# Performance work log

Hardware: AMD Instinct MI355X
Metric: run time of the kernel (lower is better)

## Reference

```python
import jax, jax.numpy as jnp
import numpy as np

B, L, C, D, M = 64, 256, 8, 512, 512


def setup_inputs() -> dict:
    key = jax.random.key(0)
    ks = jax.random.split(key, 12)
    sd = 1.0 / np.sqrt(D)
    sm = 1.0 / np.sqrt(M)
    return {
        "x": jax.random.normal(ks[0], (B, L, D), jnp.float32),
        "x_c": jax.random.randint(ks[1], (B, L, C), 0, L),
        "x_m": jax.random.uniform(ks[2], (B, L), jnp.float32),
        "x_m_c": jax.random.uniform(ks[3], (B, L, C), jnp.float32),
        "W_ioux": jax.random.uniform(ks[4], (3 * M, D), jnp.float32, -sd, sd),
        "b_ioux": jax.random.uniform(ks[5], (3 * M,), jnp.float32, -sd, sd),
        "W_iouh": jax.random.uniform(ks[6], (3 * M, M), jnp.float32, -sm, sm),
        "b_iouh": jax.random.uniform(ks[7], (3 * M,), jnp.float32, -sm, sm),
        "W_fx": jax.random.uniform(ks[8], (M, D), jnp.float32, -sd, sd),
        "b_fx": jax.random.uniform(ks[9], (M,), jnp.float32, -sd, sd),
        "W_fh": jax.random.uniform(ks[10], (M, M), jnp.float32, -sm, sm),
        "b_fh": jax.random.uniform(ks[11], (M,), jnp.float32, -sm, sm),
    }


def reference(x, x_c, x_m, x_m_c, W_ioux, b_ioux, W_iouh, b_iouh, W_fx, b_fx, W_fh, b_fh):
    bsz, len_seq, in_dim = x.shape
    mem = W_fx.shape[0]
    outputs0 = jnp.zeros((bsz, len_seq, 2 * mem), x.dtype)  # row 0 = init_state = zeros
    prev0 = jnp.zeros((bsz, 2 * mem), x.dtype)
    # time-major streams for steps 1..L-1
    xs = (
        jnp.arange(1, len_seq),
        jnp.swapaxes(x, 0, 1)[1:],
        jnp.swapaxes(x_c, 0, 1)[1:],
        jnp.swapaxes(x_m, 0, 1)[1:],
        jnp.swapaxes(x_m_c, 0, 1)[1:],
    )

    def step(carry, inputs):
        outputs, prev = carry
        t, x_t, xc_t, xm_t, xmc_t = inputs
        # gather child states [B, C, 2M] from outputs buffer
        idx = jnp.broadcast_to(xc_t[:, :, None], (bsz, xc_t.shape[1], 2 * mem))
        child = jnp.take_along_axis(outputs, idx, axis=1)
        c_s, c_h = child[..., :mem], child[..., mem:]
        mc = xmc_t[..., None]  # [B, C, 1]
        child_h_sum = jnp.sum(c_h * mc, axis=1)  # [B, M]
        iou = x_t @ W_ioux.T + b_ioux + child_h_sum @ W_iouh.T + b_iouh
        i, o, u = jnp.split(iou, 3, axis=-1)
        i, o, u = jax.nn.sigmoid(i), jax.nn.sigmoid(o), jnp.tanh(u)
        f = jax.nn.sigmoid(c_h @ W_fh.T + b_fh + (x_t @ W_fx.T + b_fx)[:, None, :])
        c = i * u + jnp.sum(f * c_s * mc, axis=1)
        h = o * jnp.tanh(c)
        s = jnp.concatenate([c, h], axis=-1)
        m = xm_t[:, None]
        s = m * s + (1.0 - m) * prev
        outputs = jax.lax.dynamic_update_slice(outputs, s[:, None, :], (0, t, 0))
        return (outputs, s), None

    (outputs, final_state), _ = jax.lax.scan(step, (outputs0, prev0), xs)
    return outputs, final_state
```

## Files before the change

### kernel.cpp

```cpp
#include <hip/hip_runtime.h>
#include <math.h>

namespace {

constexpr int Bn = 64, Ln = 256, Cn = 8, Dn = 512, Mn = 512;
constexpr int TWO_M = 2 * Mn;
constexpr int PCOLS = 2048;
constexpr size_t P_FLOATS = (size_t)Bn * Ln * PCOLS;
constexpr size_t P_BYTES  = P_FLOATS * 4;

__device__ __forceinline__ float sigmoidf_(float v) { return 1.0f / (1.0f + __expf(-v)); }
__device__ __forceinline__ float dot4_(float4 a, float4 b) {
    return a.x * b.x + a.y * b.y + a.z * b.z + a.w * b.w;
}

constexpr int PJLD = 36;

__global__ __launch_bounds__(256)
void proj2_kernel(const float* __restrict__ x,
                  const float* __restrict__ W_ioux, const float* __restrict__ b_ioux,
                  const float* __restrict__ b_iouh,
                  const float* __restrict__ W_fx, const float* __restrict__ b_fx,
                  float* __restrict__ P)
{
    __shared__ float sA[64 * PJLD];
    __shared__ float sB[64 * PJLD];
    const int tid = threadIdx.x;
    const int rb = blockIdx.x >> 5;
    const int cb = blockIdx.x & 31;
    const int r0 = rb * 64, c0 = cb * 64;
    const bool is_iou = (c0 < 3 * Mn);
    const int ri = tid & 15, ci = tid >> 4;

    float acc[4][4];
    #pragma unroll
    for (int r = 0; r < 4; ++r)
        #pragma unroll
        for (int c = 0; c < 4; ++c) acc[r][c] = 0.f;

    for (int k0 = 0; k0 < Dn; k0 += 32) {
        #pragma unroll
        for (int i = 0; i < 2; ++i) {
            const int flat = i * 256 + tid;
            const int row = flat >> 3, kq = flat & 7;
            *(float4*)&sA[row * PJLD + kq * 4] =
                *(const float4*)&x[(size_t)(r0 + row) * Dn + k0 + kq * 4];
            const float* wsrc = is_iou ? &W_ioux[(size_t)(c0 + row) * Dn]
                                       : &W_fx[(size_t)(c0 - 3 * Mn + row) * Dn];
            *(float4*)&sB[row * PJLD + kq * 4] = *(const float4*)&wsrc[k0 + kq * 4];
        }
        __syncthreads();
        #pragma unroll
        for (int k4 = 0; k4 < 8; ++k4) {
            float4 av[4], bv[4];
            #pragma unroll
            for (int r = 0; r < 4; ++r) av[r] = *(const float4*)&sA[(ri + r * 16) * PJLD + k4 * 4];
            #pragma unroll
            for (int c = 0; c < 4; ++c) bv[c] = *(const float4*)&sB[(ci + c * 16) * PJLD + k4 * 4];
            #pragma unroll
            for (int r = 0; r < 4; ++r)
                #pragma unroll
                for (int c = 0; c < 4; ++c) acc[r][c] += dot4_(av[r], bv[c]);
        }
        __syncthreads();
    }
    #pragma unroll
    for (int c = 0; c < 4; ++c) {
        const int col = c0 + ci + c * 16;
        const float bias = is_iou ? (b_ioux[col] + b_iouh[col]) : b_fx[col - 3 * Mn];
        #pragma unroll
        for (int r = 0; r < 4; ++r)
            P[(size_t)(r0 + ri + r * 16) * PCOLS + col] = acc[r][c] + bias;
    }
}

constexpr int R_W2  = 0;
constexpr int R_W1  = R_W2 + 8192;
constexpr int R_HS  = R_W1 + 24576;
constexpr int R_FD  = R_HS + 4096;
constexpr int R_IO  = R_FD + 1024;
constexpr int R_CS  = R_IO + 384;
constexpr int R_PV  = R_CS + 1024;
constexpr int R_XMC = R_PV + 256;
constexpr int R_XM  = R_XMC + 64;
constexpr int R_RB  = R_XM + 8;
constexpr int R_FLOATS = R_RB + 64;
constexpr size_t R_LDS_BYTES = (size_t)R_FLOATS * 4;
static_assert(R_LDS_BYTES <= 163840, "persist7 LDS over budget");

__global__ __launch_bounds__(512, 1)
void persist7_kernel(const int* __restrict__ x_c, const float* __restrict__ x_m,
                     const float* __restrict__ x_m_c,
                     const float* __restrict__ W_iouh, const float* __restrict__ W_fh,
                     const float* __restrict__ b_fh, const float* __restrict__ P,
                     float* __restrict__ out, unsigned* __restrict__ ctr)
{
    extern __shared__ float lds[];
    float* w2   = lds + R_W2;
    float* w1   = lds + R_W1;
    float* s_hs = lds + R_HS;
    float* s_fd = lds + R_FD;
    float* s_io = lds + R_IO;
    float* s_cs = lds + R_CS;
    float* s_pv = lds + R_PV;
    float* s_xmc = lds + R_XMC;
    float* s_xm  = lds + R_XM;
    int*   s_rb  = (int*)(lds + R_RB);

    const int tid = threadIdx.x;
    const int g  = blockIdx.x & 7;
    const int mt = blockIdx.x >> 3;
    const int m0 = mt * 16;
    const int b0 = g * 8;
    unsigned* myctr = ctr + g * 32;

    #pragma unroll
    for (int chk = 0; chk < 4; ++chk) {
        const int q = chk * 512 + tid;
        const int i = q >> 7, jj = (q >> 5) & 3, lane32 = q & 31;
        const int jh = lane32 >> 3, ks = lane32 & 7;
        *(float4*)&w2[q * 4] =
            *(const float4*)&W_fh[(size_t)(m0 + jh * 4 + jj) * Dn + ks * 4 + i * 32];
    }
    #pragma unroll
    for (int chk = 0; chk < 12; ++chk) {
        const int q = chk * 512 + tid;
        const int i = q / 384, r1 = q % 384;
        const int cc = r1 / 192, lane192 = r1 % 192;
        const int cq = lane192 >> 3, ks = lane192 & 7;
        const int col = cq * 2 + cc, s = col >> 4, j = col & 15;
        *(float4*)&w1[q * 4] =
            *(const float4*)&W_iouh[(size_t)(s * Mn + m0 + j) * Mn + ks * 4 + i * 32];
    }

    const int g2_ks = tid & 7, g2_jh = (tid >> 3) & 3, g2_rq = tid >> 5;
    const int g1_bq = tid / 192, g1_r = tid % 192;
    const int g1_cq = g1_r >> 3, g1_ks = g1_r & 7;
    const int p1_b = tid >> 6, p1_k = tid & 63;

    const float bfh_j = b_fh[m0 + (tid & 15)];
    if (tid < 256) s_pv[tid] = 0.f;

    int   sc_idx = 0;  float sc_xmc = 0.f, sc_xm = 0.f;
    float p0 = 0.f, p1 = 0.f, p2 = 0.f, p3 = 0.f;
    if (tid < 64) {
        const int b = tid >> 3, c = tid & 7;
        sc_idx = x_c[((size_t)(b0 + b) * Ln + 1) * Cn + c];
        sc_xmc = x_m_c[((size_t)(b0 + b) * Ln + 1) * Cn + c];
    } else if (tid < 72) {
        sc_xm = x_m[(size_t)(b0 + tid - 64) * Ln + 1];
    }
    if (tid < 128) {
        const size_t prow = ((size_t)(b0 + (tid >> 4)) * Ln + 1) * (size_t)PCOLS
                            + m0 + (tid & 15);
        p0 = P[prow];           p1 = P[prow + Mn];
        p2 = P[prow + 2 * Mn];  p3 = P[prow + 3 * Mn];
    }
    __syncthreads();

    for (int t = 1; t < Ln; ++t) {
        if (tid < 64) {
            const int ci = (sc_idx < t) ? sc_idx : 0;
            s_xmc[tid] = sc_xmc;
            s_rb[tid]  = ((b0 + (tid >> 3)) * Ln + ci) * TWO_M;
        } else if (tid < 72) {
            s_xm[tid - 64] = sc_xm;
        }
        __syncthreads();

        {
            const float* rowp[8];
            float wt[8];
            #pragma unroll
            for (int c = 0; c < 8; ++c) {
                rowp[c] = &out[(size_t)s_rb[p1_b * 8 + c] + Mn];
                wt[c]   = s_xmc[p1_b * 8 + c];
            }
            #pragma unroll
            for (int i = 0; i < 2; ++i) {
                const int k = p1_k * 4 + i * 256;
                float4 hs = make_float4(0.f, 0.f, 0.f, 0.f);
                #pragma unroll
                for (int c = 0; c < 8; ++c) {
                    const float4 v = *(const float4*)&rowp[c][k];
                    hs.x += wt[c] * v.x; hs.y += wt[c] * v.y;
                    hs.z += wt[c] * v.z; hs.w += wt[c] * v.w;
                }
                *(float4*)&s_hs[p1_b * 512 + k] = hs;
            }
        }
        if (tid < 256) {
            const int row = tid >> 2, q = tid & 3;
            const float4 v = *(const float4*)&out[(size_t)s_rb[row] + m0 + q * 4];
            *(float4*)&s_cs[row * 16 + q * 4] = v;
        }

        {
            const float* rp[4];
            #pragma unroll
            for (int r = 0; r < 4; ++r)
                rp[r] = &out[(size_t)s_rb[g2_rq * 4 + r] + Mn];
            float acc[4][4];
            #pragma unroll
            for (int r = 0; r < 4; ++r)
                #pragma unroll
                for (int jj = 0; jj < 4; ++jj) acc[r][jj] = 0.f;
            #pragma unroll 4
            for (int i = 0; i < 16; ++i) {
                const int k = g2_ks * 4 + i * 32;
                float4 cv[4], wv[4];
                #pragma unroll
                for (int r = 0; r < 4; ++r) cv[r] = *(const float4*)&rp[r][k];
                #pragma unroll
                for (int jj = 0; jj < 4; ++jj)
                    wv[jj] = *(const float4*)&w2[(i * 128 + jj * 32 + g2_jh * 8 + g2_ks) * 4];
                #pragma unroll
                for (int r = 0; r < 4; ++r)
                    #pragma unroll
                    for (int jj = 0; jj < 4; ++jj) acc[r][jj] += dot4_(cv[r], wv[jj]);
            }
            #pragma unroll
            for (int r = 0; r < 4; ++r)
                #pragma unroll
                for (int jj = 0; jj < 4; ++jj) {
                    float v = acc[r][jj];
                    v += __shfl_xor(v, 1); v += __shfl_xor(v, 2); v += __shfl_xor(v, 4);
                    acc[r][jj] = v;
                }
            if (g2_ks == 0) {
                #pragma unroll
                for (int r = 0; r < 4; ++r)
                    *(float4*)&s_fd[(g2_rq * 4 + r) * 16 + g2_jh * 4] =
                        make_float4(acc[r][0], acc[r][1], acc[r][2], acc[r][3]);
            }
        }
        __syncthreads();

        if (tid < 384) {
            float acc[2][4];
            #pragma unroll
            for (int cc = 0; cc < 2; ++cc)
                #pragma unroll
                for (int bb = 0; bb < 4; ++bb) acc[cc][bb] = 0.f;
            #pragma unroll 4
            for (int i = 0; i < 16; ++i) {
                const int k = g1_ks * 4 + i * 32;
                float4 hv[4];
                #pragma unroll
                for (int bb = 0; bb < 4; ++bb)
                    hv[bb] = *(const float4*)&s_hs[(g1_bq * 4 + bb) * 512 + k];
                #pragma unroll
                for (int cc = 0; cc < 2; ++cc) {
                    const float4 wv = *(const float4*)&w1[((i * 2 + cc) * 192
                                                           + g1_cq * 8 + g1_ks) * 4];
                    #pragma unroll
                    for (int bb = 0; bb < 4; ++bb) acc[cc][bb] += dot4_(hv[bb], wv);
                }
            }
            #pragma unroll
            for (int cc = 0; cc < 2; ++cc)
                #pragma unroll
                for (int bb = 0; bb < 4; ++bb) {
                    float v = acc[cc][bb];
                    v += __shfl_xor(v, 1); v += __shfl_xor(v, 2); v += __shfl_xor(v, 4);
                    acc[cc][bb] = v;
                }
            if (g1_ks == 0) {
                #pragma unroll
                for (int cc = 0; cc < 2; ++cc)
                    #pragma unroll
                    for (int bb = 0; bb < 4; ++bb)
                        s_io[(g1_bq * 4 + bb) * 48 + g1_cq * 2 + cc] = acc[cc][bb];
            }
        }

        int   nx_idx = 0;  float nx_xmc = 0.f, nx_xm = 0.f;
        float np0 = 0.f, np1 = 0.f, np2 = 0.f, np3 = 0.f;
        if (t < Ln - 1) {
            const int tn = t + 1;
            if (tid < 64) {
                const int b = tid >> 3, c = tid & 7;
                nx_idx = x_c[((size_t)(b0 + b) * Ln + tn) * Cn + c];
                nx_xmc = x_m_c[((size_t)(b0 + b) * Ln + tn) * Cn + c];
            } else if (tid < 72) {
                nx_xm = x_m[(size_t)(b0 + tid - 64) * Ln + tn];
            }
            if (tid < 128) {
                const size_t prow = ((size_t)(b0 + (tid >> 4)) * Ln + tn) * (size_t)PCOLS
                                    + m0 + (tid & 15);
                np0 = P[prow];           np1 = P[prow + Mn];
                np2 = P[prow + 2 * Mn];  np3 = P[prow + 3 * Mn];
            }
        }
        __syncthreads();

        if (tid < 128) {
            const int b = tid >> 4, j = tid & 15;
            const float iv = s_io[b * 48 + j]      + p0;
            const float ov = s_io[b * 48 + 16 + j] + p1;
            const float uv = s_io[b * 48 + 32 + j] + p2;
            const float i_ = sigmoidf_(iv);
            const float o_ = sigmoidf_(ov);
            const float u_ = tanhf(uv);
            float facc = 0.f;
            #pragma unroll
            for (int c = 0; c < 8; ++c) {
                const int row = b * 8 + c;
                const float f = sigmoidf_(s_fd[row * 16 + j] + bfh_j + p3);
                facc += f * s_cs[row * 16 + j] * s_xmc[row];
            }
            const float cv = i_ * u_ + facc;
            const float hv = o_ * tanhf(cv);
            const float mv = s_xm[b];
            const float nc = mv * cv + (1.f - mv) * s_pv[b * 32 + j];
            const float nh = mv * hv + (1.f - mv) * s_pv[b * 32 + 16 + j];
            const size_t ob = ((size_t)(b0 + b) * Ln + t) * TWO_M;
            out[ob + m0 + j]      = nc;
            out[ob + Mn + m0 + j] = nh;
            s_pv[b * 32 + j]      = nc;
            s_pv[b * 32 + 16 + j] = nh;
        }
        __syncthreads();

        if (t < Ln - 1) {
            if (tid == 0) {
                __hip_atomic_fetch_add(myctr, 1u, __ATOMIC_RELEASE, __HIP_MEMORY_SCOPE_AGENT);
                const unsigned target = 32u * (unsigned)t;
                while (__hip_atomic_load(myctr, __ATOMIC_RELAXED, __HIP_MEMORY_SCOPE_AGENT) < target)
                    __builtin_amdgcn_s_sleep(2);
                (void)__hip_atomic_load(myctr, __ATOMIC_ACQUIRE, __HIP_MEMORY_SCOPE_AGENT);
            }
            __syncthreads();
        }
        sc_idx = nx_idx; sc_xmc = nx_xmc; sc_xm = nx_xm;
        p0 = np0; p1 = np1; p2 = np2; p3 = np3;
    }
}

constexpr int LBT = 4, LMT = 32, LNMT = Mn / LMT, LPAD = 4, LDK = Dn + LPAD;
constexpr int L_U16 = 4096, L_CHS = LBT * LDK, L_CH = LBT * Cn * LDK,
              L_WFH = LMT * LDK, L_CS = LBT * Cn * LMT, L_IOUF = 4 * LBT * LMT;
constexpr int L_FLOATS = L_U16 + L_CHS + L_CH + L_WFH + L_CS + L_IOUF + 32 + 4 + 32;
constexpr size_t L_BYTES = (size_t)L_FLOATS * 4;

__global__ __launch_bounds__(256, 1)
void step_legacy(const float* __restrict__ x, const int* __restrict__ x_c,
                 const float* __restrict__ x_m, const float* __restrict__ x_m_c,
                 const float* __restrict__ W_ioux, const float* __restrict__ b_ioux,
                 const float* __restrict__ W_iouh, const float* __restrict__ b_iouh,
                 const float* __restrict__ W_fx, const float* __restrict__ b_fx,
                 const float* __restrict__ W_fh, const float* __restrict__ b_fh,
                 float* __restrict__ out, int t)
{
    extern __shared__ float lds[];
    float* u16    = lds;
    float* s_chs  = u16 + L_U16;
    float* s_ch   = s_chs + L_CHS;
    float* s_wfh  = s_ch + L_CH;
    float* s_cs   = s_wfh + L_WFH;
    float* s_iouf = s_cs + L_CS;
    float* s_xmc  = s_iouf + L_IOUF;
    float* s_xm   = s_xmc + 32;
    int*   s_xc   = (int*)(s_xm + 4);

    const int tid = threadIdx.x;
    const int mt = blockIdx.x & (LNMT - 1);
    const int bt = blockIdx.x >> 4;
    const int b0 = bt * LBT, m0 = mt * LMT;

    #pragma unroll
    for (int i = 0; i < 8; ++i) {
        int flat = i * 256 + tid, b = flat >> 9, k = flat & 511;
        u16[b * LDK + k] = x[((size_t)(b0 + b) * Ln + t) * Dn + k];
    }
    if (tid < 32) {
        int b = tid >> 3, c = tid & 7;
        s_xc[tid]  = x_c[((size_t)(b0 + b) * Ln + t) * Cn + c];
        s_xmc[tid] = x_m_c[((size_t)(b0 + b) * Ln + t) * Cn + c];
    }
    if (tid < 4) s_xm[tid] = x_m[(size_t)(b0 + tid) * Ln + t];
    for (int i = 0; i < 64; ++i) {
        int flat = i * 256 + tid, j = flat >> 9, k = flat & 511;
        s_wfh[j * LDK + k] = W_fh[(size_t)(m0 + j) * Dn + k];
    }
    __syncthreads();

    #pragma unroll
    for (int i = 0; i < 8; ++i) {
        int flat = i * 256 + tid, b = flat >> 9, k = flat & 511;
        float acc = 0.f;
        #pragma unroll
        for (int c = 0; c < 8; ++c) {
            int idx = s_xc[b * 8 + c];
            float v = 0.f;
            if (idx < t) v = out[((size_t)(b0 + b) * Ln + idx) * TWO_M + Mn + k];
            s_ch[(b * 8 + c) * LDK + k] = v;
            acc += s_xmc[b * 8 + c] * v;
        }
        s_chs[b * LDK + k] = acc;
    }
    #pragma unroll
    for (int i = 0; i < 4; ++i) {
        int flat = i * 256 + tid;
        int b = flat >> 8, rem = flat & 255, c = rem >> 5, j = rem & 31;
        int idx = s_xc[b * 8 + c];
        float v = 0.f;
        if (idx < t) v = out[((size_t)(b0 + b) * Ln + idx) * TWO_M + m0 + j];
        s_cs[flat] = v;
    }
    __syncthreads();

    {
        const int unit = tid >> 3, ksl = tid & 7, s = unit >> 3, jg = unit & 7;
        float acc[4][4];
        #pragma unroll
        for (int b = 0; b < 4; ++b)
            #pragma unroll
            for (int jj = 0; jj < 4; ++jj) acc[b][jj] = 0.f;
        if (s < 3) {
            const int colbase = s * Mn + m0 + jg * 4;
            #pragma unroll 4
            for (int it = 0; it < 16; ++it) {
                const int k = it * 32 + ksl * 4;
                float4 sx[4], sc[4];
                #pragma unroll
                for (int b = 0; b < 4; ++b) {
                    sx[b] = *(const float4*)&u16[b * LDK + k];
                    sc[b] = *(const float4*)&s_chs[b * LDK + k];
                }
                #pragma unroll
                for (int jj = 0; jj < 4; ++jj) {
                    const float4 wx = *(const float4*)&W_ioux[(size_t)(colbase + jj) * Dn + k];
                    const float4 wh = *(const float4*)&W_iouh[(size_t)(colbase + jj) * Dn + k];
                    #pragma unroll
                    for (int b = 0; b < 4; ++b)
                        acc[b][jj] += dot4_(sx[b], wx) + dot4_(sc[b], wh);
                }
            }
        } else {
            const int colbase = m0 + jg * 4;
            #pragma unroll 4
            for (int it = 0; it < 16; ++it) {
                const int k = it * 32 + ksl * 4;
                float4 sx[4];
                #pragma unroll
                for (int b = 0; b < 4; ++b) sx[b] = *(const float4*)&u16[b * LDK + k];
                #pragma unroll
                for (int jj = 0; jj < 4; ++jj) {
                    const float4 wx = *(const float4*)&W_fx[(size_t)(colbase + jj) * Dn + k];
                    #pragma unroll
                    for (int b = 0; b < 4; ++b) acc[b][jj] += dot4_(sx[b], wx);
                }
            }
        }
        __syncthreads();
        #pragma unroll
        for (int b = 0; b < 4; ++b)
            #pragma unroll
            for (int jj = 0; jj < 4; ++jj)
                u16[unit * 128 + ksl * 16 + b * 4 + jj] = acc[b][jj];
        __syncthreads();
        #pragma unroll
        for (int e = 0; e < 2; ++e) {
            const int task = e * 256 + tid;
            const int unit2 = task >> 4, rem = task & 15;
            float v = 0.f;
            #pragma unroll
            for (int k2 = 0; k2 < 8; ++k2) v += u16[unit2 * 128 + k2 * 16 + rem];
            const int s2 = unit2 >> 3, jg2 = unit2 & 7;
            const int bb = rem >> 2, jj = rem & 3, j = jg2 * 4 + jj;
            float bias = (s2 < 3) ? (b_ioux[s2 * Mn + m0 + j] + b_iouh[s2 * Mn + m0 + j])
                                  : b_fx[m0 + j];
            s_iouf[(s2 * 4 + bb) * 32 + j] = v + bias;
        }
    }
    __syncthreads();

    {
        const int pos = tid >> 2, ksc = tid & 3, rg = pos >> 3, jg = pos & 7;
        float acc[4][4];
        #pragma unroll
        for (int r = 0; r < 4; ++r)
            #pragma unroll
            for (int j = 0; j < 4; ++j) acc[r][j] = 0.f;
        #pragma unroll 4
        for (int it = 0; it < 32; ++it) {
            const int k = it * 16 + ksc * 4;
            float4 ch[4], wf[4];
            #pragma unroll
            for (int r = 0; r < 4; ++r) ch[r] = *(const float4*)&s_ch[(rg * 4 + r) * LDK + k];
            #pragma unroll
            for (int j = 0; j < 4; ++j) wf[j] = *(const float4*)&s_wfh[(jg * 4 + j) * LDK + k];
            #pragma unroll
            for (int r = 0; r < 4; ++r)
                #pragma unroll
                for (int j = 0; j < 4; ++j) acc[r][j] += dot4_(ch[r], wf[j]);
        }
        #pragma unroll
        for (int r = 0; r < 4; ++r)
            #pragma unroll
            for (int j = 0; j < 4; ++j)
                u16[((rg * 4 + r) * 32 + (jg * 4 + j)) * 4 + ksc] = acc[r][j];
    }
    __syncthreads();

    if (tid < 128) {
        const int b = tid >> 5, j = tid & 31;
        const float iv  = s_iouf[(0 * 4 + b) * 32 + j];
        const float ov  = s_iouf[(1 * 4 + b) * 32 + j];
        const float uv  = s_iouf[(2 * 4 + b) * 32 + j];
        const float fxv = s_iouf[(3 * 4 + b) * 32 + j];
        const float i_ = sigmoidf_(iv), o_ = sigmoidf_(ov), u_ = tanhf(uv);
        const float bfh = b_fh[m0 + j];
        float facc = 0.f;
        #pragma unroll
        for (int c = 0; c < 8; ++c) {
            const int row = b * 8 + c;
            const float fd = u16[(row * 32 + j) * 4 + 0] + u16[(row * 32 + j) * 4 + 1]
                           + u16[(row * 32 + j) * 4 + 2] + u16[(row * 32 + j) * 4 + 3];
            const float f = sigmoidf_(fd + bfh + fxv);
            facc += f * s_cs[row * 32 + j] * s_xmc[row];
        }
        const float cval = i_ * u_ + facc;
        const float hval = o_ * tanhf(cval);
        const float mval = s_xm[b];
        const size_t base  = ((size_t)(b0 + b) * Ln + t) * TWO_M;
        const size_t pbase = ((size_t)(b0 + b) * Ln + (t - 1)) * TWO_M;
        out[base + m0 + j]      = mval * cval + (1.f - mval) * out[pbase + m0 + j];
        out[base + Mn + m0 + j] = mval * hval + (1.f - mval) * out[pbase + Mn + m0 + j];
    }
}

__global__ void zero_row0(float* __restrict__ out) {
    int i = blockIdx.x * 256 + threadIdx.x;
    int b = i >> 10, j = i & 1023;
    out[(size_t)b * Ln * TWO_M + j] = 0.f;
}

__global__ void zero_ctr(unsigned* __restrict__ c) {
    if (threadIdx.x < 8) c[threadIdx.x * 32] = 0u;
}

__global__ void final_copy(const float* __restrict__ out, float* __restrict__ fin) {
    int i = blockIdx.x * 256 + threadIdx.x;
    int b = i >> 10, j = i & 1023;
    fin[i] = out[((size_t)b * Ln + (Ln - 1)) * TWO_M + j];
}

}

extern "C" void kernel_launch(void* const* d_in, const int* in_sizes, int n_in,
                              void* d_out, int out_size, void* d_ws, size_t ws_size,
                              hipStream_t stream) {
    (void)in_sizes; (void)n_in; (void)out_size;
    const float* x      = (const float*)d_in[0];
    const int*   x_c    = (const int*)d_in[1];
    const float* x_m    = (const float*)d_in[2];
    const float* x_m_c  = (const float*)d_in[3];
    const float* W_ioux = (const float*)d_in[4];
    const float* b_ioux = (const float*)d_in[5];
    const float* W_iouh = (const float*)d_in[6];
    const float* b_iouh = (const float*)d_in[7];
    const float* W_fx   = (const float*)d_in[8];
    const float* b_fx   = (const float*)d_in[9];
    const float* W_fh   = (const float*)d_in[10];
    const float* b_fh   = (const float*)d_in[11];
    float* out = (float*)d_out;
    float* fin = out + (size_t)Bn * Ln * TWO_M;

    hipFuncSetAttribute((const void*)persist7_kernel,
                        hipFuncAttributeMaxDynamicSharedMemorySize, (int)R_LDS_BYTES);
    hipFuncSetAttribute((const void*)step_legacy,
                        hipFuncAttributeMaxDynamicSharedMemorySize, (int)L_BYTES);

    hipLaunchKernelGGL(zero_row0, dim3(256), dim3(256), 0, stream, out);

    if (ws_size >= P_BYTES) {
        float* Pp = (float*)d_ws;
        unsigned* ctr = (unsigned*)d_ws;
        hipLaunchKernelGGL(proj2_kernel, dim3(8192), dim3(256), 0, stream,
                           x, W_ioux, b_ioux, b_iouh, W_fx, b_fx, Pp);
        hipLaunchKernelGGL(zero_ctr, dim3(1), dim3(64), 0, stream, ctr);
        void* kargs[] = { (void*)&x_c, (void*)&x_m, (void*)&x_m_c, (void*)&W_iouh,
                          (void*)&W_fh, (void*)&b_fh, (void*)&Pp, (void*)&out,
                          (void*)&ctr };
        hipLaunchCooperativeKernel((const void*)persist7_kernel, dim3(256), dim3(512),
                                   kargs, (unsigned)R_LDS_BYTES, stream);
    } else {
        for (int t = 1; t < Ln; ++t) {
            hipLaunchKernelGGL(step_legacy, dim3(256), dim3(256), L_BYTES, stream,
                               x, x_c, x_m, x_m_c, W_ioux, b_ioux, W_iouh, b_iouh,
                               W_fx, b_fx, W_fh, b_fh, out, t);
        }
    }
    hipLaunchKernelGGL(final_copy, dim3(256), dim3(256), 0, stream, out, fin);
}
```

Baseline: 5.045 ms.

## Replace per-step group barrier with dependency-driven progress flags

Each block now publishes its completed step in a per-block progress slot instead of incrementing a shared counter and waiting for all 32 blocks every step. Before the next step, the block computes the maximum child timestep actually referenced by its batch group and waits only when that exceeds the step it already waited for, polling all 32 slots in parallel. The aim is to skip most inter-block barriers, since child indices are often far in the past. The cost is a warp reduction per step and a correctness dependency on the child-index analysis, because only child rows, not the previous row, are read from global memory. The P workspace is aliased with the counters, though the same aliasing existed before.

```diff
diff --git a/kernel.cpp b/kernel.cpp
--- a/kernel.cpp
+++ b/kernel.cpp
@@ -84,16 +84,17 @@
 constexpr int R_XMC = R_PV + 256;
 constexpr int R_XM  = R_XMC + 64;
 constexpr int R_RB  = R_XM + 8;
-constexpr int R_FLOATS = R_RB + 64;
+constexpr int R_TN  = R_RB + 64;
+constexpr int R_FLOATS = R_TN + 4;
 constexpr size_t R_LDS_BYTES = (size_t)R_FLOATS * 4;
-static_assert(R_LDS_BYTES <= 163840, "persist7 LDS over budget");
+static_assert(R_LDS_BYTES <= 163840, "persist11 LDS over budget");
 
 __global__ __launch_bounds__(512, 1)
-void persist7_kernel(const int* __restrict__ x_c, const float* __restrict__ x_m,
-                     const float* __restrict__ x_m_c,
-                     const float* __restrict__ W_iouh, const float* __restrict__ W_fh,
-                     const float* __restrict__ b_fh, const float* __restrict__ P,
-                     float* __restrict__ out, unsigned* __restrict__ ctr)
+void persist11_kernel(const int* __restrict__ x_c, const float* __restrict__ x_m,
+                      const float* __restrict__ x_m_c,
+                      const float* __restrict__ W_iouh, const float* __restrict__ W_fh,
+                      const float* __restrict__ b_fh, const float* __restrict__ P,
+                      float* __restrict__ out, int* __restrict__ ctr)
 {
     extern __shared__ float lds[];
     float* w2   = lds + R_W2;
@@ -106,13 +107,14 @@
     float* s_xmc = lds + R_XMC;
     float* s_xm  = lds + R_XM;
     int*   s_rb  = (int*)(lds + R_RB);
+    int*   s_tn  = (int*)(lds + R_TN);
 
     const int tid = threadIdx.x;
     const int g  = blockIdx.x & 7;
     const int mt = blockIdx.x >> 3;
     const int m0 = mt * 16;
     const int b0 = g * 8;
-    unsigned* myctr = ctr + g * 32;
+    int* prog = ctr + g * 32;
 
     #pragma unroll
     for (int chk = 0; chk < 4; ++chk) {
@@ -156,6 +158,7 @@
         p0 = P[prow];           p1 = P[prow + Mn];
         p2 = P[prow + 2 * Mn];  p3 = P[prow + 3 * Mn];
     }
+    int last_wait = 0;
     __syncthreads();
 
     for (int t = 1; t < Ln; ++t) {
@@ -282,6 +285,13 @@
                 const int b = tid >> 3, c = tid & 7;
                 nx_idx = x_c[((size_t)(b0 + b) * Ln + tn) * Cn + c];
                 nx_xmc = x_m_c[((size_t)(b0 + b) * Ln + tn) * Cn + c];
+                int eff = (nx_idx < tn) ? nx_idx : 0;
+                #pragma unroll
+                for (int m = 1; m <= 32; m <<= 1) {
+                    const int o = __shfl_xor(eff, m);
+                    eff = (o > eff) ? o : eff;
+                }
+                if (tid == 0) s_tn[0] = eff;
             } else if (tid < 72) {
                 nx_xm = x_m[(size_t)(b0 + tid - 64) * Ln + tn];
             }
@@ -293,6 +303,9 @@
             }
         }
         __syncthreads();
+
+        const int  tn_val  = s_tn[0];
+        const bool anyneed = (t < Ln - 1) && (tn_val > last_wait);
 
         if (tid < 128) {
             const int b = tid >> 4, j = tid & 15;
@@ -323,14 +336,18 @@
         __syncthreads();
 
         if (t < Ln - 1) {
-            if (tid == 0) {
-                __hip_atomic_fetch_add(myctr, 1u, __ATOMIC_RELEASE, __HIP_MEMORY_SCOPE_AGENT);
-                const unsigned target = 32u * (unsigned)t;
-                while (__hip_atomic_load(myctr, __ATOMIC_RELAXED, __HIP_MEMORY_SCOPE_AGENT) < target)
-                    __builtin_amdgcn_s_sleep(2);
-                (void)__hip_atomic_load(myctr, __ATOMIC_ACQUIRE, __HIP_MEMORY_SCOPE_AGENT);
-            }
-            __syncthreads();
+            if (tid == 0)
+                __hip_atomic_store(&prog[mt], t, __ATOMIC_RELEASE, __HIP_MEMORY_SCOPE_AGENT);
+            if (anyneed) {
+                if (tid < 32) {
+                    while (__hip_atomic_load(&prog[tid], __ATOMIC_RELAXED,
+                                             __HIP_MEMORY_SCOPE_AGENT) < tn_val)
+                        __builtin_amdgcn_s_sleep(2);
+                }
+                __builtin_amdgcn_fence(__ATOMIC_ACQUIRE, "agent");
+                __syncthreads();
+                last_wait = tn_val;
+            }
         }
         sc_idx = nx_idx; sc_xmc = nx_xmc; sc_xm = nx_xm;
         p0 = np0; p1 = np1; p2 = np2; p3 = np3;
@@ -537,8 +554,8 @@
     out[(size_t)b * Ln * TWO_M + j] = 0.f;
 }
 
-__global__ void zero_ctr(unsigned* __restrict__ c) {
-    if (threadIdx.x < 8) c[threadIdx.x * 32] = 0u;
+__global__ void zero_ctr(int* __restrict__ c) {
+    c[threadIdx.x] = 0;
 }
 
 __global__ void final_copy(const float* __restrict__ out, float* __restrict__ fin) {
@@ -568,7 +585,7 @@
     float* out = (float*)d_out;
     float* fin = out + (size_t)Bn * Ln * TWO_M;
 
-    hipFuncSetAttribute((const void*)persist7_kernel,
+    hipFuncSetAttribute((const void*)persist11_kernel,
                         hipFuncAttributeMaxDynamicSharedMemorySize, (int)R_LDS_BYTES);
     hipFuncSetAttribute((const void*)step_legacy,
                         hipFuncAttributeMaxDynamicSharedMemorySize, (int)L_BYTES);
@@ -577,14 +594,14 @@
 
     if (ws_size >= P_BYTES) {
         float* Pp = (float*)d_ws;
-        unsigned* ctr = (unsigned*)d_ws;
+        int* ctr = (int*)d_ws;
         hipLaunchKernelGGL(proj2_kernel, dim3(8192), dim3(256), 0, stream,
                            x, W_ioux, b_ioux, b_iouh, W_fx, b_fx, Pp);
-        hipLaunchKernelGGL(zero_ctr, dim3(1), dim3(64), 0, stream, ctr);
+        hipLaunchKernelGGL(zero_ctr, dim3(1), dim3(256), 0, stream, ctr);
         void* kargs[] = { (void*)&x_c, (void*)&x_m, (void*)&x_m_c, (void*)&W_iouh,
                           (void*)&W_fh, (void*)&b_fh, (void*)&Pp, (void*)&out,
                           (void*)&ctr };
-        hipLaunchCooperativeKernel((const void*)persist7_kernel, dim3(256), dim3(512),
+        hipLaunchCooperativeKernel((const void*)persist11_kernel, dim3(256), dim3(512),
                                    kargs, (unsigned)R_LDS_BYTES, stream);
     } else {
         for (int t = 1; t < Ln; ++t) {
```

Result: slower. 5.989 ms (+18.7%).
